# Kernel tuning notes

Measured on AMD Instinct MI355X. Metric: run time of the kernel, lower is better.

Reference implementation:

```python
import jax, jax.numpy as jnp
import numpy as np

C, Q, F, N = 50000, 8, 256, 65536  # num_classes, instances/class, feat_len, n_proposals


def setup_inputs() -> dict:
    key = jax.random.key(0)
    kf, kl = jax.random.split(key)
    return {
        "features": jax.random.normal(kf, (N, F), jnp.float32),
        "queue": jnp.zeros((C, Q, F), jnp.float32),
        "pid_labels": jax.random.randint(kl, (N,), 0, C, jnp.int32),
        "tail": jnp.zeros((C,), jnp.int32),
    }


def _update(features, queue, pid_labels, tail):
    # Parallel-equivalent of the sequential per-label circular-buffer write:
    # proposal i with label l writes to slot (tail[l] + occ_i) % Q where occ_i is
    n = features.shape[0]
    c, q, f = queue.shape
    valid = (pid_labels >= 0) & (pid_labels < c)
    lab = jnp.where(valid, pid_labels, c)  # sentinel c for invalid labels
    order = jnp.argsort(lab)  # stable sort groups equal labels, preserves order
    sl = lab[order]
    first = jnp.searchsorted(sl, sl, side="left").astype(lab.dtype)
    occ_sorted = jnp.arange(n, dtype=lab.dtype) - first  # occurrence index within label group
    occ = jnp.zeros(n, lab.dtype).at[order].set(occ_sorted)
    lab_c = jnp.clip(lab, 0, c - 1)
    slot = (tail[lab_c].astype(lab.dtype) + occ) % q
    flat = jnp.where(valid, lab_c * q + slot, 0)  # flat (class, slot) bucket
    writer = jnp.where(valid, jnp.arange(n, dtype=jnp.int32), -1)
    last = jax.ops.segment_max(writer, flat, num_segments=c * q)  # last proposal hitting each bucket
    written = last >= 0
    qf = jnp.where(written[:, None], features[jnp.clip(last, 0)], queue.reshape(c * q, f))
    return qf.reshape(c, q, f)


def reference(features, queue, pid_labels, tail):
    return _update(features, queue, pid_labels, tail)
```

## Files before the change

kernel.cpp:

```cpp
#include <hip/hip_runtime.h>


typedef float vf4 __attribute__((ext_vector_type(4)));

#define HBLK 1024

__global__ void k_hist(const int* __restrict__ lab, int* __restrict__ cnt,
                       int N, int C) {
    int b = blockIdx.x;
    int t = threadIdx.x;
    int* row = cnt + (size_t)b * C;
    for (int j = t; j < C; j += HBLK) row[j] = 0;
    __syncthreads();
    int i = b * HBLK + t;
    if (i < N) {
        int l = lab[i];
        if (l >= 0 && l < C) atomicAdd(&row[l], 1);
    }
}

__global__ void k_prefix(int* __restrict__ cnt, int* __restrict__ ktot,
                         int* __restrict__ idx, int C, int NB, int Q) {
    int l = blockIdx.x * blockDim.x + threadIdx.x;
    if (l >= C) return;
    int run = 0;
    for (int b = 0; b < NB; ++b) {
        int t = cnt[(size_t)b * C + l];
        cnt[(size_t)b * C + l] = run;
        run += t;
    }
    ktot[l] = run;
    for (int q = 0; q < Q; ++q) idx[l * Q + q] = -1;
}

__global__ void k_slots(const int* __restrict__ lab, const int* __restrict__ tail,
                        const int* __restrict__ cnt, const int* __restrict__ ktot,
                        int* __restrict__ idx, int N, int C, int Q) {
    __shared__ int slab[HBLK];
    int b = blockIdx.x;
    int t = threadIdx.x;
    int i = b * HBLK + t;
    int l = (i < N) ? lab[i] : -1;
    slab[t] = l;
    __syncthreads();
    if (l < 0 || l >= C) return;
    int local = 0;
    for (int j = 0; j < t; ++j) local += (slab[j] == l) ? 1 : 0;
    int occ = cnt[(size_t)b * C + l] + local;
    int kk = ktot[l];
    if (occ >= kk - Q) {
        int s = (tail[l] + occ) % Q;
        if (s < 0) s += Q;
        idx[l * Q + s] = i;
    }
}

__global__ void k_gather(const vf4* __restrict__ feat,
                         const vf4* __restrict__ queue,
                         const int* __restrict__ idx,
                         vf4* __restrict__ out,
                         long long total4, int F4) {
    long long stride = (long long)gridDim.x * blockDim.x;
    if (F4 == 64) {
        for (long long g = (long long)blockIdx.x * blockDim.x + threadIdx.x;
             g < total4; g += stride) {
            int r = (int)(g >> 6);
            int c = (int)(g & 63);
            int id = idx[r];
            const vf4* src = (id >= 0) ? (feat + ((size_t)id << 6) + c)
                                       : (queue + ((size_t)r << 6) + c);
            vf4 v = __builtin_nontemporal_load(src);
            __builtin_nontemporal_store(v, &out[g]);
        }
    } else {
        for (long long g = (long long)blockIdx.x * blockDim.x + threadIdx.x;
             g < total4; g += stride) {
            int r = (int)(g / F4);
            int c = (int)(g - (long long)r * F4);
            int id = idx[r];
            const vf4* src = (id >= 0) ? (feat + (size_t)id * F4 + c)
                                       : (queue + (size_t)r * F4 + c);
            vf4 v = __builtin_nontemporal_load(src);
            __builtin_nontemporal_store(v, &out[g]);
        }
    }
}

extern "C" void kernel_launch(void* const* d_in, const int* in_sizes, int n_in,
                              void* d_out, int out_size, void* d_ws, size_t ws_size,
                              hipStream_t stream) {
    const float* feat  = (const float*)d_in[0];
    const float* queue = (const float*)d_in[1];
    const int*   lab   = (const int*)d_in[2];
    const int*   tail  = (const int*)d_in[3];

    const int N = in_sizes[2];
    const int C = in_sizes[3];
    const int F = in_sizes[0] / N;
    const int Q = in_sizes[1] / (C * F);
    const int NB = (N + HBLK - 1) / HBLK;

    int* idx  = (int*)d_ws;
    int* cnt  = idx + (size_t)C * Q;
    int* ktot = cnt + (size_t)NB * C;

    k_hist<<<NB, HBLK, 0, stream>>>(lab, cnt, N, C);
    k_prefix<<<(C + 255) / 256, 256, 0, stream>>>(cnt, ktot, idx, C, NB, Q);
    k_slots<<<NB, HBLK, 0, stream>>>(lab, tail, cnt, ktot, idx, N, C, Q);

    const int F4 = F / 4;
    const long long total4 = (long long)C * Q * F4;
    int gblocks = 2048;
    long long need = (total4 + 255) / 256;
    if (need < gblocks) gblocks = (int)need;
    k_gather<<<gblocks, 256, 0, stream>>>((const vf4*)feat,
                                          (const vf4*)queue, idx,
                                          (vf4*)d_out, total4, F4);
}
```

Baseline: 192.2 us.

## Split zeroing into vectorized kernel, vectorize slot counting, unroll gather by two

Adds a dedicated k_zero kernel that clears the count table and sets idx to -1 with 16-byte stores, replacing the per-block zeroing in k_hist and the scalar idx init in k_prefix. k_hist now runs with 256-thread blocks and atomics straight to global memory. The within-block occurrence scan in k_slots reads shared memory four ints at a time. The gather loop is unrolled by two to keep more loads in flight. k_zero assumes C*Q and NB*C are multiples of 4, otherwise leftover elements are never initialized.

After: 199.8 us. 3.9% more time.

```diff
diff --git a/kernel.cpp b/kernel.cpp
--- a/kernel.cpp
+++ b/kernel.cpp
@@ -2,25 +2,33 @@
 
 
 typedef float vf4 __attribute__((ext_vector_type(4)));
+typedef int   vi4 __attribute__((ext_vector_type(4)));
 
 #define HBLK 1024
 
+__global__ void k_zero(int* __restrict__ idx, long long nIdx,
+                       int* __restrict__ cnt, long long nCnt) {
+    long long stride = (long long)gridDim.x * blockDim.x;
+    long long g0 = (long long)blockIdx.x * blockDim.x + threadIdx.x;
+    vi4* idx4 = (vi4*)idx;
+    vi4* cnt4 = (vi4*)cnt;
+    vi4 mone; mone.x = mone.y = mone.z = mone.w = -1;
+    vi4 zero; zero.x = zero.y = zero.z = zero.w = 0;
+    for (long long g = g0; g < nIdx / 4; g += stride) idx4[g] = mone;
+    for (long long g = g0; g < nCnt / 4; g += stride) cnt4[g] = zero;
+}
+
 __global__ void k_hist(const int* __restrict__ lab, int* __restrict__ cnt,
                        int N, int C) {
-    int b = blockIdx.x;
-    int t = threadIdx.x;
-    int* row = cnt + (size_t)b * C;
-    for (int j = t; j < C; j += HBLK) row[j] = 0;
-    __syncthreads();
-    int i = b * HBLK + t;
+    int i = blockIdx.x * blockDim.x + threadIdx.x;
     if (i < N) {
         int l = lab[i];
-        if (l >= 0 && l < C) atomicAdd(&row[l], 1);
+        if (l >= 0 && l < C) atomicAdd(&cnt[(size_t)(i >> 10) * C + l], 1);
     }
 }
 
 __global__ void k_prefix(int* __restrict__ cnt, int* __restrict__ ktot,
-                         int* __restrict__ idx, int C, int NB, int Q) {
+                         int C, int NB) {
     int l = blockIdx.x * blockDim.x + threadIdx.x;
     if (l >= C) return;
     int run = 0;
@@ -30,13 +38,12 @@
         run += t;
     }
     ktot[l] = run;
-    for (int q = 0; q < Q; ++q) idx[l * Q + q] = -1;
 }
 
 __global__ void k_slots(const int* __restrict__ lab, const int* __restrict__ tail,
                         const int* __restrict__ cnt, const int* __restrict__ ktot,
                         int* __restrict__ idx, int N, int C, int Q) {
-    __shared__ int slab[HBLK];
+    __shared__ __align__(16) int slab[HBLK];
     int b = blockIdx.x;
     int t = threadIdx.x;
     int i = b * HBLK + t;
@@ -44,8 +51,14 @@
     slab[t] = l;
     __syncthreads();
     if (l < 0 || l >= C) return;
+    const vi4* slab4 = (const vi4*)slab;
     int local = 0;
-    for (int j = 0; j < t; ++j) local += (slab[j] == l) ? 1 : 0;
+    int nw = t >> 2;
+    for (int w = 0; w < nw; ++w) {
+        vi4 v = slab4[w];
+        local += (v.x == l) + (v.y == l) + (v.z == l) + (v.w == l);
+    }
+    for (int j = t & ~3; j < t; ++j) local += (slab[j] == l);
     int occ = cnt[(size_t)b * C + l] + local;
     int kk = ktot[l];
     if (occ >= kk - Q) {
@@ -61,26 +74,39 @@
                          vf4* __restrict__ out,
                          long long total4, int F4) {
     long long stride = (long long)gridDim.x * blockDim.x;
+    long long g = (long long)blockIdx.x * blockDim.x + threadIdx.x;
     if (F4 == 64) {
-        for (long long g = (long long)blockIdx.x * blockDim.x + threadIdx.x;
-             g < total4; g += stride) {
-            int r = (int)(g >> 6);
-            int c = (int)(g & 63);
+        for (; g + stride < total4; g += 2 * stride) {
+            long long g2 = g + stride;
+            int r1 = (int)(g >> 6),  c1 = (int)(g & 63);
+            int r2 = (int)(g2 >> 6), c2 = (int)(g2 & 63);
+            int id1 = idx[r1];
+            int id2 = idx[r2];
+            const vf4* s1 = (id1 >= 0) ? (feat + ((size_t)id1 << 6) + c1)
+                                       : (queue + ((size_t)r1 << 6) + c1);
+            const vf4* s2 = (id2 >= 0) ? (feat + ((size_t)id2 << 6) + c2)
+                                       : (queue + ((size_t)r2 << 6) + c2);
+            vf4 v1 = __builtin_nontemporal_load(s1);
+            vf4 v2 = __builtin_nontemporal_load(s2);
+            __builtin_nontemporal_store(v1, &out[g]);
+            __builtin_nontemporal_store(v2, &out[g2]);
+        }
+        if (g < total4) {
+            int r = (int)(g >> 6), c = (int)(g & 63);
             int id = idx[r];
-            const vf4* src = (id >= 0) ? (feat + ((size_t)id << 6) + c)
-                                       : (queue + ((size_t)r << 6) + c);
-            vf4 v = __builtin_nontemporal_load(src);
+            const vf4* s = (id >= 0) ? (feat + ((size_t)id << 6) + c)
+                                     : (queue + ((size_t)r << 6) + c);
+            vf4 v = __builtin_nontemporal_load(s);
             __builtin_nontemporal_store(v, &out[g]);
         }
     } else {
-        for (long long g = (long long)blockIdx.x * blockDim.x + threadIdx.x;
-             g < total4; g += stride) {
+        for (; g < total4; g += stride) {
             int r = (int)(g / F4);
             int c = (int)(g - (long long)r * F4);
             int id = idx[r];
-            const vf4* src = (id >= 0) ? (feat + (size_t)id * F4 + c)
-                                       : (queue + (size_t)r * F4 + c);
-            vf4 v = __builtin_nontemporal_load(src);
+            const vf4* s = (id >= 0) ? (feat + (size_t)id * F4 + c)
+                                     : (queue + (size_t)r * F4 + c);
+            vf4 v = __builtin_nontemporal_load(s);
             __builtin_nontemporal_store(v, &out[g]);
         }
     }
@@ -104,12 +130,14 @@
     int* cnt  = idx + (size_t)C * Q;
     int* ktot = cnt + (size_t)NB * C;
 
-    k_hist<<<NB, HBLK, 0, stream>>>(lab, cnt, N, C);
-    k_prefix<<<(C + 255) / 256, 256, 0, stream>>>(cnt, ktot, idx, C, NB, Q);
+    const long long R = (long long)C * Q;
+    k_zero<<<2048, 256, 0, stream>>>(idx, R, cnt, (long long)NB * C);
+    k_hist<<<(N + 255) / 256, 256, 0, stream>>>(lab, cnt, N, C);
+    k_prefix<<<(C + 255) / 256, 256, 0, stream>>>(cnt, ktot, C, NB);
     k_slots<<<NB, HBLK, 0, stream>>>(lab, tail, cnt, ktot, idx, N, C, Q);
 
     const int F4 = F / 4;
-    const long long total4 = (long long)C * Q * F4;
+    const long long total4 = R * F4;
     int gblocks = 2048;
     long long need = (total4 + 255) / 256;
     if (need < gblocks) gblocks = (int)need;
```
